# Performance work log

Measured on AMD Instinct MI355X. Metric: run time of the kernel, lower is better.

Reference implementation:

```python
import jax, jax.numpy as jnp
import numpy as np

B, N, C, H, D, K = 4, 8192, 384, 12, 2, 256
M = N // K          # 32 members per cluster
CH = C // H         # 32 head dim


def setup_inputs() -> dict:
    key = jax.random.key(0)
    ks = jax.random.split(key, 8)
    pos = jax.random.uniform(ks[0], (B, N, D), jnp.float32) * 100.0
    feat = jax.random.normal(ks[1], (B, N, C), jnp.float32)
    # each batch's points partitioned into K clusters of M members (a permutation)
    perms = jax.vmap(lambda kk: jax.random.permutation(kk, N))(jax.random.split(ks[2], B))
    member_idx = perms.reshape(B * K, M).astype(jnp.int32)               # z x m
    batch_idx = jnp.broadcast_to(
        jnp.repeat(jnp.arange(B, dtype=jnp.int32), K)[:, None], (B * K, M))
    w = 0.02
    qkv_w = jax.random.normal(ks[3], (3 * C, C), jnp.float32) * w
    qkv_b = jnp.zeros((3 * C,), jnp.float32)
    pos_w = jax.random.normal(ks[4], (H, D), jnp.float32) * w
    pos_b = jnp.zeros((H,), jnp.float32)
    proj_w = jax.random.normal(ks[5], (C, C), jnp.float32) * w
    proj_b = jnp.zeros((C,), jnp.float32)
    return dict(pos=pos, feat=feat, member_idx=member_idx, batch_idx=batch_idx,
                qkv_w=qkv_w, qkv_b=qkv_b, pos_w=pos_w, pos_b=pos_b,
                proj_w=proj_w, proj_b=proj_b, k=K)


def reference(pos, feat, member_idx, batch_idx, qkv_w, qkv_b, pos_w, pos_b,
              proj_w, proj_b, k):
    # attend_means=True, mask=None, cluster_score=None, q_subsample_idx=None path
    b, n, c = feat.shape
    d = pos.shape[2]
    h = pos_w.shape[0]
    ch = c // h
    z, m = member_idx.shape
    scale = ch ** -0.5

    qkv = feat @ qkv_w.T + qkv_b            # b,n,3c
    q = qkv[..., :c]                        # b,n,c
    kv = qkv[..., c:]                       # b,n,2c

    pos_orig = pos
    pos_n = pos / jnp.max(pos.reshape(-1, d), axis=0)   # per-coordinate max norm

    # irregular gather of kv / pos per cluster member
    kv_g = kv[batch_idx, member_idx]        # z,m,2c
    pos_g = pos_n[batch_idx, member_idx]    # z,m,d

    # cluster_score=None, mask=None -> uniform weights 1/m (mean over members)
    kv_mean = jnp.mean(kv_g, axis=1).reshape(b, k, 2, h, ch)
    pos_mean = jnp.mean(pos_g, axis=1).reshape(b, k, d)

    key_ = kv_mean[:, :, 0].transpose(0, 2, 1, 3)   # b,h,k,ch
    v = kv_mean[:, :, 1].transpose(0, 2, 1, 3)      # b,h,k,ch
    qh = q.reshape(b, n, h, ch).transpose(0, 2, 1, 3) * scale  # b,h,n,ch

    attn = jnp.einsum('bhnc,bhkc->bhnk', qh, key_)  # b,h,n,k
    rel_pos = pos_mean[:, None, :, :] - pos_orig[:, :, None, :]  # b,n,k,d
    pos_bias = jnp.einsum('bnkd,hd->bhnk', rel_pos, pos_w) + pos_b[None, :, None, None]
    attn = jax.nn.softmax(attn + pos_bias, axis=-1)

    out = jnp.einsum('bhnk,bhkc->bnhc', attn, v).reshape(b, n, c)
    return out @ proj_w.T + proj_b
```

## Files before the change

kernel.cpp:

```cpp
#include <hip/hip_runtime.h>

typedef __attribute__((ext_vector_type(8))) short bf16x8;
typedef __attribute__((ext_vector_type(4))) float f32x4;

#define MFMA16(a,b,c) __builtin_amdgcn_mfma_f32_16x16x32_bf16((a),(b),(c),0,0,0)

__device__ __forceinline__ float b2f(unsigned short u){
  union { unsigned u; float f; } x; x.u = ((unsigned)u) << 16; return x.f;
}
__device__ __forceinline__ unsigned short f2b(float f){
  union { float f; unsigned u; } x; x.f = f;
  unsigned r = x.u + 0x7FFFu + ((x.u >> 16) & 1u);
  return (unsigned short)(r >> 16);
}
__device__ __forceinline__ unsigned pk_rne(float a, float b){
  unsigned ua = __float_as_uint(a), ub = __float_as_uint(b);
  ua += 0x7FFFu + ((ua >> 16) & 1u);
  ub += 0x7FFFu + ((ub >> 16) & 1u);
  return __builtin_amdgcn_perm(ub, ua, 0x07060302u);
}
__device__ __forceinline__ unsigned pk_trunc(float a, float b){
  return __builtin_amdgcn_perm(__float_as_uint(b), __float_as_uint(a), 0x07060302u);
}
__device__ __forceinline__ bf16x8 mk8(unsigned a, unsigned b, unsigned c, unsigned d){
  union { uint4 u; bf16x8 h; } x; x.u = make_uint4(a,b,c,d); return x.h;
}
__device__ __forceinline__ int permp(int cl){
  return (cl & 0xE0) | (((cl >> 2) & 3) << 3) | (((cl >> 4) & 1) << 2) | (cl & 3);
}

typedef __attribute__((address_space(3))) unsigned int lds_u32;
typedef const __attribute__((address_space(1))) unsigned int glb_u32;
__device__ __forceinline__ void gl_lds16(const void* g, void* l){
  __builtin_amdgcn_global_load_lds((glb_u32*)g, (lds_u32*)l, 16, 0, 0);
}

__global__ __launch_bounds__(192) void prep_means_kernel(
    const float* __restrict__ pos, unsigned* __restrict__ pmax,
    const float* __restrict__ qkv_w, unsigned short* __restrict__ qkvwb,
    const float* __restrict__ proj_w, unsigned short* __restrict__ projwb,
    const float* __restrict__ feat,
    const int* __restrict__ member_idx, const int* __restrict__ batch_idx,
    unsigned short* __restrict__ fm, float* __restrict__ pm,
    unsigned short* __restrict__ featb)
{
  int bid = blockIdx.x, t = threadIdx.x;
  if (bid < 1024){
    int g = t / 96, tl = t - g*96;
    int z = bid;
    __shared__ int bases[32];
    __shared__ float4 part[96];
    if (t < 32) bases[t] = batch_idx[z*32 + t]*8192 + member_idx[z*32 + t];
    __syncthreads();
    if (t < 32){
      float2 pp = ((const float2*)pos)[bases[t]];
      #pragma unroll
      for (int off = 16; off >= 1; off >>= 1){
        pp.x += __shfl_xor(pp.x, off, 32);
        pp.y += __shfl_xor(pp.y, off, 32);
      }
      if (t == 0){ pm[z*2] = pp.x*(1.f/32.f); pm[z*2+1] = pp.y*(1.f/32.f); }
    }
    float4 v[16]; int rows[16];
    const float4* f4 = (const float4*)feat;
    #pragma unroll
    for (int m = 0; m < 16; m++){
      rows[m] = bases[g*16 + m];
      v[m] = f4[(long)rows[m]*96 + tl];
    }
    float4 a = {0.f,0.f,0.f,0.f};
    #pragma unroll
    for (int m = 0; m < 16; m++){
      *(uint2*)(featb + (long)rows[m]*384 + tl*4) =
          make_uint2(pk_rne(v[m].x, v[m].y), pk_rne(v[m].z, v[m].w));
      a.x += v[m].x; a.y += v[m].y; a.z += v[m].z; a.w += v[m].w;
    }
    if (g == 1) part[tl] = a;
    __syncthreads();
    if (g == 0){
      float4 b = part[tl];
      a.x += b.x; a.y += b.y; a.z += b.z; a.w += b.w;
      unsigned d0 = pk_rne(a.x*(1.f/32.f), a.y*(1.f/32.f));
      unsigned d1 = pk_rne(a.z*(1.f/32.f), a.w*(1.f/32.f));
      *(uint2*)(fm + (long)z*384 + tl*4) = make_uint2(d0, d1);
    }
  } else if (bid < 1408){
    int u = (bid - 1024)*192 + t;
    const float* in; unsigned short* o; long i;
    if (u < 55296){ in = qkv_w;  o = qkvwb;  i = u; }
    else          { in = proj_w; o = projwb; i = u - 55296; }
    const float4* p = (const float4*)(in + i*8);
    float4 a = p[0], b = p[1];
    *(uint4*)(o + i*8) = make_uint4(pk_rne(a.x,a.y), pk_rne(a.z,a.w),
                                    pk_rne(b.x,b.y), pk_rne(b.z,b.w));
  } else {
    int i = (bid - 1408)*192 + t;
    if (i < 16384){
      float4 v = ((const float4*)pos)[i];
      float m0 = fmaxf(v.x, v.z), m1 = fmaxf(v.y, v.w);
      #pragma unroll
      for (int off = 32; off >= 1; off >>= 1){
        m0 = fmaxf(m0, __shfl_xor(m0, off, 64));
        m1 = fmaxf(m1, __shfl_xor(m1, off, 64));
      }
      if ((t & 63) == 0){
        atomicMax(&pmax[0], __float_as_uint(m0));
        atomicMax(&pmax[1], __float_as_uint(m1));
      }
    }
  }
}

__global__ __launch_bounds__(512) void kvq_kernel(
    const unsigned short* __restrict__ fm,
    const unsigned short* __restrict__ featb,
    const unsigned short* __restrict__ qkvwb,
    const float* __restrict__ qkv_b,
    const float* __restrict__ pm, const float* __restrict__ pmaxf,
    const float* __restrict__ pos_w, const float* __restrict__ pos_b,
    unsigned short* __restrict__ kh, unsigned short* __restrict__ vt,
    unsigned short* __restrict__ wt,
    unsigned short* __restrict__ q_s, float q_scale)
{
  __shared__ unsigned short As[64*64];
  __shared__ unsigned short Ws[384*64];
  __shared__ unsigned short wtS[256];
  const int K = 384;
  int tid = threadIdx.x;
  int lane = tid & 63, wave = tid >> 6;
  int l15 = lane & 15, quad = lane >> 4;
  int sw = l15 & 7;
  int srow = tid >> 3, sc8 = tid & 7;

  int qtile;
  if (blockIdx.x < 96){
    int mt = blockIdx.x / 6, nt = blockIdx.x - mt*6;
    int m0 = mt << 6, n0 = nt << 7;
    int b = m0 >> 8, cl0 = m0 & 255;
    const unsigned short* W = qkvwb + 384*384;
    if (nt >= 3 && tid < 256){
      int lh = tid >> 6, lc = tid & 63;
      int h = ((n0 - 384) >> 5) + lh;
      int cl = cl0 + lc;
      float p0 = pm[(b*256 + cl)*2]   / pmaxf[0];
      float p1 = pm[(b*256 + cl)*2+1] / pmaxf[1];
      float bias = p0*pos_w[h*2] + p1*pos_w[h*2+1] + pos_b[h];
      unsigned short wv = f2b(exp2f(bias * 1.44269504088896340f));
      wtS[lh*64 + lc] = wv;
      wt[(((long)(b*12 + h)) << 8) + permp(cl)] = wv;
    }
    int wr = (wave >> 2) << 5, wc = (wave & 3) << 5;
    f32x4 acc[2][2];
    #pragma unroll
    for (int i = 0; i < 2; i++)
      #pragma unroll
      for (int j = 0; j < 2; j++) acc[i][j] = (f32x4){0.f,0.f,0.f,0.f};

    for (int k0 = 0; k0 < K; k0 += 64){
      __syncthreads();
      int gc8 = sc8 ^ (srow & 7);
      gl_lds16(fm + (long)(m0+srow)*K + k0 + gc8*8, As + wave*512);
      #pragma unroll
      for (int it = 0; it < 2; it++){
        int r = it*64 + srow;
        int g2 = sc8 ^ (r & 7);
        gl_lds16(W + (long)(n0+r)*K + k0 + g2*8, Ws + it*4096 + wave*512);
      }
      __syncthreads();
      #pragma unroll
      for (int kk = 0; kk < 2; kk++){
        bf16x8 af[2], bfr[2];
        #pragma unroll
        for (int i = 0; i < 2; i++)
          af[i] = *(const bf16x8*)(As + (wr + i*16 + l15)*64 + (((kk<<2)+quad) ^ sw)*8);
        #pragma unroll
        for (int j = 0; j < 2; j++)
          bfr[j] = *(const bf16x8*)(Ws + (wc + j*16 + l15)*64 + (((kk<<2)+quad) ^ sw)*8);
        #pragma unroll
        for (int i = 0; i < 2; i++)
          #pragma unroll
          for (int j = 0; j < 2; j++)
            acc[i][j] = MFMA16(af[i], bfr[j], acc[i][j]);
      }
    }

    #pragma unroll
    for (int j = 0; j < 2; j++){
      int col = n0 + wc + j*16 + l15;
      float bv = qkv_b[384 + col];
      #pragma unroll
      for (int i = 0; i < 2; i++){
        #pragma unroll
        for (int r = 0; r < 4; r++){
          float v = acc[i][j][r] + bv;
          int lr = wr + i*16 + quad*4 + r;
          int cl = cl0 + lr;
          if (col < 384){
            int h = col >> 5, ch = col & 31;
            kh[((((long)b*12 + h)*256 + cl)*32) + ch] = f2b(v);
          } else {
            int cn = col - 384;
            int h = cn >> 5, ch = cn & 31;
            int pp = permp(cl);
            int c8 = (pp >> 3) ^ (ch & 7);
            float w = b2f(wtS[(wave & 3)*64 + lr]);
            vt[(((long)b*12 + h)*32 + ch)*256 + c8*8 + (pp & 7)] = f2b(v * w);
          }
        }
      }
    }
    qtile = 416 + blockIdx.x;
  } else {
    qtile = blockIdx.x - 96;
  }

  {
    int m0 = qtile << 6;
    f32x4 acc[4][3];
    #pragma unroll
    for (int i = 0; i < 4; i++)
      #pragma unroll
      for (int j = 0; j < 3; j++) acc[i][j] = (f32x4){0.f,0.f,0.f,0.f};

    for (int k0 = 0; k0 < K; k0 += 64){
      __syncthreads();
      int gc8 = sc8 ^ (srow & 7);
      gl_lds16(featb + (long)(m0+srow)*K + k0 + gc8*8, As + wave*512);
      #pragma unroll
      for (int it = 0; it < 6; it++){
        int r = it*64 + srow;
        int g2 = sc8 ^ (r & 7);
        gl_lds16(qkvwb + (long)r*K + k0 + g2*8, Ws + it*4096 + wave*512);
      }
      __syncthreads();
      #pragma unroll
      for (int kk = 0; kk < 2; kk++){
        bf16x8 af[4];
        #pragma unroll
        for (int i = 0; i < 4; i++)
          af[i] = *(const bf16x8*)(As + (i*16 + l15)*64 + (((kk<<2)+quad) ^ sw)*8);
        #pragma unroll
        for (int j = 0; j < 3; j++){
          bf16x8 bfr = *(const bf16x8*)(Ws + (wave*48 + j*16 + l15)*64 + (((kk<<2)+quad) ^ sw)*8);
          #pragma unroll
          for (int i = 0; i < 4; i++)
            acc[i][j] = MFMA16(af[i], bfr, acc[i][j]);
        }
      }
    }

    #pragma unroll
    for (int j = 0; j < 3; j++){
      int col = wave*48 + j*16 + l15;
      float bv = qkv_b[col];
      #pragma unroll
      for (int i = 0; i < 4; i++){
        int row0 = m0 + i*16 + quad*4;
        #pragma unroll
        for (int r = 0; r < 4; r++){
          float v = (acc[i][j][r] + bv) * q_scale;
          int row = row0 + r;
          int bb = row >> 13, tok = row & 8191;
          q_s[((((long)(bb*12 + (col >> 5))) << 13) + tok)*32 + (col & 31)] = f2b(v);
        }
      }
    }
  }
}

__global__ __launch_bounds__(512, 4) void attnproj_kernel(
    const unsigned short* __restrict__ qhm,
    const unsigned short* __restrict__ kh,
    const unsigned short* __restrict__ vt,
    const unsigned short* __restrict__ wt,
    const unsigned short* __restrict__ projwb,
    const float* __restrict__ proj_b,
    float* __restrict__ out)
{
  __shared__ unsigned short oS[2][64*64];

  int bid = blockIdx.x;
  int b = bid >> 7;
  int t0 = (bid & 127) << 6;
  int tid = threadIdx.x, lane = tid & 63, wave = tid >> 6;
  int l15 = lane & 15, quad = lane >> 4;
  int sw = l15 & 7;
  int hsel = wave >> 2, ti = wave & 3;

  f32x4 acc[4][3];
  #pragma unroll
  for (int i = 0; i < 4; i++)
    #pragma unroll
    for (int j = 0; j < 3; j++) acc[i][j] = (f32x4){0.f,0.f,0.f,0.f};

  for (int it = 0; it < 6; it++){
    int head = 2*it + hsel;
    long bh = (long)b*12 + head;
    const unsigned short* kb = kh + bh*8192;
    const unsigned short* vb = vt + bh*8192;
    const unsigned short* wb = wt + bh*256;

    bf16x8 aq = *(const bf16x8*)(qhm + (bh*8192 + t0 + ti*16 + l15)*32 + quad*8);

    f32x4 o0 = {0.f,0.f,0.f,0.f}, o1 = {0.f,0.f,0.f,0.f}, os = {0.f,0.f,0.f,0.f};
    #pragma unroll
    for (int ks8 = 0; ks8 < 8; ks8++){
      bf16x8 bk0 = *(const bf16x8*)(kb + (32*ks8 + l15)*32 + quad*8);
      bf16x8 bk1 = *(const bf16x8*)(kb + (32*ks8 + 16 + l15)*32 + quad*8);
      const f32x4 z4 = {0.f,0.f,0.f,0.f};
      f32x4 s0 = MFMA16(bk0, aq, z4);
      f32x4 s1 = MFMA16(bk1, aq, z4);
      #pragma unroll
      for (int c = 0; c < 4; c++){ s0[c] = exp2f(s0[c]); s1[c] = exp2f(s1[c]); }
      bf16x8 pf = mk8(pk_trunc(s0[0],s0[1]), pk_trunc(s0[2],s0[3]),
                      pk_trunc(s1[0],s1[1]), pk_trunc(s1[2],s1[3]));
      int c8 = (4*ks8 + quad) ^ sw;
      bf16x8 a0 = *(const bf16x8*)(vb + l15*256      + c8*8);
      bf16x8 a1 = *(const bf16x8*)(vb + (16+l15)*256 + c8*8);
      bf16x8 wf = *(const bf16x8*)(wb + ks8*32 + quad*8);
      o0 = MFMA16(a0, pf, o0);
      o1 = MFMA16(a1, pf, o1);
      os = MFMA16(wf, pf, os);
    }

    float inv = 1.f / os[0];
    unsigned short* ob = &oS[it & 1][0];
    int tokLoc = ti*16 + l15;
    int oct0 = hsel*4 + (quad >> 1);
    int wi = (quad & 1)*4;
    *(uint2*)(ob + tokLoc*64 + ((oct0 ^ sw)*8 + wi)) =
        make_uint2(pk_rne(o0[0]*inv, o0[1]*inv), pk_rne(o0[2]*inv, o0[3]*inv));
    *(uint2*)(ob + tokLoc*64 + (((oct0+2) ^ sw)*8 + wi)) =
        make_uint2(pk_rne(o1[0]*inv, o1[1]*inv), pk_rne(o1[2]*inv, o1[3]*inv));
    __syncthreads();

    #pragma unroll
    for (int kk = 0; kk < 2; kk++){
      bf16x8 af[4];
      #pragma unroll
      for (int i = 0; i < 4; i++)
        af[i] = *(const bf16x8*)(ob + (i*16 + l15)*64 + (((kk<<2)+quad) ^ sw)*8);
      #pragma unroll
      for (int j = 0; j < 3; j++){
        bf16x8 bfr = *(const bf16x8*)(projwb + (long)(wave*48 + j*16 + l15)*384
                                      + it*64 + (kk*4 + quad)*8);
        #pragma unroll
        for (int i = 0; i < 4; i++)
          acc[i][j] = MFMA16(af[i], bfr, acc[i][j]);
      }
    }
  }

  #pragma unroll
  for (int j = 0; j < 3; j++){
    int col = wave*48 + j*16 + l15;
    float bv = proj_b[col];
    #pragma unroll
    for (int i = 0; i < 4; i++){
      long row0 = (long)b*8192 + t0 + i*16 + quad*4;
      #pragma unroll
      for (int r = 0; r < 4; r++)
        out[(row0 + r)*384 + col] = acc[i][j][r] + bv;
    }
  }
}

extern "C" void kernel_launch(void* const* d_in, const int* in_sizes, int n_in,
                              void* d_out, int out_size, void* d_ws, size_t ws_size,
                              hipStream_t stream)
{
  const float* pos      = (const float*)d_in[0];
  const float* feat     = (const float*)d_in[1];
  const int* member_idx = (const int*)d_in[2];
  const int* batch_idx  = (const int*)d_in[3];
  const float* qkv_w    = (const float*)d_in[4];
  const float* qkv_b    = (const float*)d_in[5];
  const float* pos_w    = (const float*)d_in[6];
  const float* pos_b    = (const float*)d_in[7];
  const float* proj_w   = (const float*)d_in[8];
  const float* proj_b   = (const float*)d_in[9];
  float* out = (float*)d_out;

  char* ws = (char*)d_ws;
  float* pmax           = (float*)ws;
  float* pm             = (float*)(ws + 256);
  unsigned short* fm    = (unsigned short*)(ws + 8704);
  unsigned short* kh    = (unsigned short*)(ws + 795136);
  unsigned short* vt    = (unsigned short*)(ws + 1581568);
  unsigned short* wt    = (unsigned short*)(ws + 2368000);
  unsigned short* q_s   = (unsigned short*)(ws + 2417152);
  unsigned short* qkvwb = (unsigned short*)(ws + 52748800);
  unsigned short* projwb= (unsigned short*)(ws + 53633536);
  unsigned short* featb = (unsigned short*)(ws + 53928448);

  hipMemsetAsync(pmax, 0, 8, stream);
  prep_means_kernel<<<1494, 192, 0, stream>>>(pos, (unsigned*)pmax, qkv_w, qkvwb,
                                              proj_w, projwb, feat, member_idx,
                                              batch_idx, fm, pm, featb);
  kvq_kernel<<<512, 512, 0, stream>>>(fm, featb, qkvwb, qkv_b, pm, pmax, pos_w, pos_b,
                                      kh, vt, wt, q_s,
                                      0.17677669529663687f * 1.44269504088896340f);
  attnproj_kernel<<<512, 512, 0, stream>>>(q_s, kh, vt, wt, projwb, proj_b, out);
}
```

Measured before the change: 214.7 us.

## Stage key/value tiles in double-buffered LDS and process one head per iteration

The attention+projection kernel now uses 256 threads per block and loops over all 12 heads one at a time. It prefetches each head's key, value-transpose and weight-sum tiles into double-buffered shared memory through async global-to-LDS copies, so the next head loads while the current one computes. Each wave now covers 96 output columns instead of 48, which doubles the accumulator registers. Shared memory use grows to about 66KB per block, which may limit occupancy. The swizzle on the output staging buffer is replaced by a padded stride of 40.

```diff
diff --git a/kernel.cpp b/kernel.cpp
--- a/kernel.cpp
+++ b/kernel.cpp
@@ -268,7 +268,7 @@
   }
 }
 
-__global__ __launch_bounds__(512, 4) void attnproj_kernel(
+__global__ __launch_bounds__(256, 2) void attnproj_kernel(
     const unsigned short* __restrict__ qhm,
     const unsigned short* __restrict__ kh,
     const unsigned short* __restrict__ vt,
@@ -277,7 +277,10 @@
     const float* __restrict__ proj_b,
     float* __restrict__ out)
 {
-  __shared__ unsigned short oS[2][64*64];
+  __shared__ unsigned short keyS[2][8192];
+  __shared__ unsigned short vTS[2][8192];
+  __shared__ unsigned short wS[2][256];
+  __shared__ unsigned short oS[2][64*40];
 
   int bid = blockIdx.x;
   int b = bid >> 7;
@@ -285,22 +288,38 @@
   int tid = threadIdx.x, lane = tid & 63, wave = tid >> 6;
   int l15 = lane & 15, quad = lane >> 4;
   int sw = l15 & 7;
-  int hsel = wave >> 2, ti = wave & 3;
-
-  f32x4 acc[4][3];
+  long bbase = (long)b*12;
+
+  f32x4 acc[4][6];
   #pragma unroll
   for (int i = 0; i < 4; i++)
     #pragma unroll
-    for (int j = 0; j < 3; j++) acc[i][j] = (f32x4){0.f,0.f,0.f,0.f};
-
-  for (int it = 0; it < 6; it++){
-    int head = 2*it + hsel;
-    long bh = (long)b*12 + head;
-    const unsigned short* kb = kh + bh*8192;
-    const unsigned short* vb = vt + bh*8192;
-    const unsigned short* wb = wt + bh*256;
-
-    bf16x8 aq = *(const bf16x8*)(qhm + (bh*8192 + t0 + ti*16 + l15)*32 + quad*8);
+    for (int j = 0; j < 6; j++) acc[i][j] = (f32x4){0.f,0.f,0.f,0.f};
+
+  auto stage = [&](int buf, int h){
+    const unsigned short* ks = kh + (bbase + h)*8192;
+    const unsigned short* vs = vt + (bbase + h)*8192;
+    #pragma unroll
+    for (int p = 0; p < 4; p++){
+      gl_lds16(ks + p*2048 + tid*8, &keyS[buf][p*2048 + wave*512]);
+      gl_lds16(vs + p*2048 + tid*8, &vTS[buf][p*2048 + wave*512]);
+    }
+    if (tid < 32) gl_lds16(wt + (bbase + h)*256 + lane*8, &wS[buf][0]);
+  };
+
+  stage(0, 0);
+  __syncthreads();
+
+  for (int it = 0; it < 12; ++it){
+    int buf = it & 1;
+    if (it < 11) stage(buf ^ 1, it + 1);
+
+    long bh = bbase + it;
+    bf16x8 aq = *(const bf16x8*)(qhm + (bh*8192 + t0 + wave*16 + l15)*32 + quad*8);
+
+    const unsigned short* kb = &keyS[buf][0];
+    const unsigned short* vb = &vTS[buf][0];
+    const unsigned short* wb = &wS[buf][0];
 
     f32x4 o0 = {0.f,0.f,0.f,0.f}, o1 = {0.f,0.f,0.f,0.f}, os = {0.f,0.f,0.f,0.f};
     #pragma unroll
@@ -324,36 +343,31 @@
     }
 
     float inv = 1.f / os[0];
-    unsigned short* ob = &oS[it & 1][0];
-    int tokLoc = ti*16 + l15;
-    int oct0 = hsel*4 + (quad >> 1);
-    int wi = (quad & 1)*4;
-    *(uint2*)(ob + tokLoc*64 + ((oct0 ^ sw)*8 + wi)) =
+    unsigned short* ob = &oS[buf][0];
+    int row = wave*16 + l15;
+    *(uint2*)(ob + row*40 + quad*4) =
         make_uint2(pk_rne(o0[0]*inv, o0[1]*inv), pk_rne(o0[2]*inv, o0[3]*inv));
-    *(uint2*)(ob + tokLoc*64 + (((oct0+2) ^ sw)*8 + wi)) =
+    *(uint2*)(ob + row*40 + 16 + quad*4) =
         make_uint2(pk_rne(o1[0]*inv, o1[1]*inv), pk_rne(o1[2]*inv, o1[3]*inv));
     __syncthreads();
 
-    #pragma unroll
-    for (int kk = 0; kk < 2; kk++){
-      bf16x8 af[4];
+    bf16x8 af[4];
+    #pragma unroll
+    for (int i = 0; i < 4; i++)
+      af[i] = *(const bf16x8*)(ob + (i*16 + l15)*40 + quad*8);
+    #pragma unroll
+    for (int j = 0; j < 6; j++){
+      int col = wave*96 + j*16 + l15;
+      bf16x8 bfr = *(const bf16x8*)(projwb + (long)col*384 + it*32 + quad*8);
       #pragma unroll
       for (int i = 0; i < 4; i++)
-        af[i] = *(const bf16x8*)(ob + (i*16 + l15)*64 + (((kk<<2)+quad) ^ sw)*8);
-      #pragma unroll
-      for (int j = 0; j < 3; j++){
-        bf16x8 bfr = *(const bf16x8*)(projwb + (long)(wave*48 + j*16 + l15)*384
-                                      + it*64 + (kk*4 + quad)*8);
-        #pragma unroll
-        for (int i = 0; i < 4; i++)
-          acc[i][j] = MFMA16(af[i], bfr, acc[i][j]);
-      }
+        acc[i][j] = MFMA16(af[i], bfr, acc[i][j]);
     }
   }
 
   #pragma unroll
-  for (int j = 0; j < 3; j++){
-    int col = wave*48 + j*16 + l15;
+  for (int j = 0; j < 6; j++){
+    int col = wave*96 + j*16 + l15;
     float bv = proj_b[col];
     #pragma unroll
     for (int i = 0; i < 4; i++){
@@ -400,5 +414,5 @@
   kvq_kernel<<<512, 512, 0, stream>>>(fm, featb, qkvwb, qkv_b, pm, pmax, pos_w, pos_b,
                                       kh, vt, wt, q_s,
                                       0.17677669529663687f * 1.44269504088896340f);
-  attnproj_kernel<<<512, 512, 0, stream>>>(q_s, kh, vt, wt, projwb, proj_b, out);
-}
+  attnproj_kernel<<<512, 256, 0, stream>>>(q_s, kh, vt, wt, projwb, proj_b, out);
+}
```

New measurement: 190.1 us. 11.5% less time.
